# Kernel tuning notes

Measured on AMD Instinct MI355X. Metric: run time of the kernel, lower is better.

## Reference

```python
import jax, jax.numpy as jnp
import numpy as np

E = 8          # num_experts
TOP_K = 2
CAP_RATIO = 1.2


def setup_inputs() -> dict:
    key = jax.random.key(0)
    k1, k2, k3, k4 = jax.random.split(key, 4)
    B, L, D, H = 2, 2048, 768, 2048
    x = jax.random.normal(k1, (B, L, D), dtype=jnp.float32)
    Wg = jax.random.normal(k2, (D, E), dtype=jnp.float32) * 0.02   # gate: Linear(D, E, bias=False)
    W1 = jax.random.normal(k3, (E, D, 2 * H), dtype=jnp.float32) * 0.02  # fc1 per expert (y | gate halves)
    W2 = jax.random.normal(k4, (E, H, D), dtype=jnp.float32) * 0.02      # fc2 per expert
    return {"x": x, "Wg": Wg, "W1": W1, "W2": W2}


def reference(x, Wg, W1, W2):
    B, L, D = x.shape
    H = W2.shape[1]
    xf = x.reshape(-1, D)                      # [N, D]
    N = xf.shape[0]
    capacity = int(CAP_RATIO * N / E)          # static, matches torch int()

    logits = xf @ Wg                           # [N, E]
    scores, idx = jax.lax.top_k(logits, TOP_K) # [N, K] (descending, like torch.topk)
    weights = jax.nn.softmax(scores, axis=-1)  # [N, K]

    # padded token table: row N is a zero token used for unfilled capacity slots
    xpad = jnp.concatenate([xf, jnp.zeros((1, D), xf.dtype)], axis=0)
    wpad_zero = jnp.zeros((1,), weights.dtype)
    out = jnp.zeros((N, D), x.dtype)

    for k in range(TOP_K):
        ik = idx[:, k]                                         # [N] expert id per token
        onehot = (ik[:, None] == jnp.arange(E)[None, :])       # [N, E]
        pos = jnp.cumsum(onehot, axis=0) - 1                   # rank within expert, ascending token order
        posk = jnp.take_along_axis(pos, ik[:, None], axis=1)[:, 0]  # [N]
        keep = posk < capacity                                 # first-come capacity (== indices[:capacity])

        # dispatch buffer [E, C]: token index per slot, N (pad) where unfilled/dropped
        buf = jnp.full((E, capacity), N, dtype=jnp.int32)
        buf = buf.at[ik, posk].set(jnp.arange(N, dtype=jnp.int32), mode="drop")

        xg = xpad[buf]                                         # [E, C, D]
        h = jnp.einsum("ecd,edh->ech", xg, W1)                 # [E, C, 2H]
        act = h[..., :H] * jax.nn.silu(h[..., H:])             # GatedMLP: y * silu(gate)
        ye = jnp.einsum("ech,ehd->ecd", act, W2)               # [E, C, D]

        wk = jnp.where(keep, weights[:, k], 0.0)               # [N]
        w_buf = jnp.concatenate([wk, wpad_zero])[buf]          # [E, C], 0 on pad slots
        out = out.at[buf.reshape(-1)].add(
            (w_buf[..., None] * ye).reshape(E * capacity, D), mode="drop"
        )

    return out.reshape(B, L, D)
```

## Files before the change

### kernel.cpp

```cpp
#include <hip/hip_runtime.h>


typedef _Float16 half8 __attribute__((ext_vector_type(8)));
typedef _Float16 half4t __attribute__((ext_vector_type(4)));
typedef float f4 __attribute__((ext_vector_type(4)));

#define N_TOK 4096
#define DDIM  768
#define HDIM  2048
#define NEXP  8
#define CAP   614
#define CAPP  640

#define XH_OFF    0L
#define W1T_OFF   6292992L
#define W2T_OFF   56624640L
#define ACT_OFF   81790464L
#define EIDX_OFF  123733504L
#define WTS_OFF   123766272L
#define TOKL_OFF  123799040L
#define CNT_OFF   123840000L

__device__ __forceinline__ void gld16(const void* g, void* l) {
  __builtin_amdgcn_global_load_lds(
      (const __attribute__((address_space(1))) unsigned int*)g,
      (__attribute__((address_space(3))) unsigned int*)l, 16, 0, 0);
}

__global__ __launch_bounds__(256) void cvt_tr_kernel(const float* __restrict__ src,
                                                     _Float16* __restrict__ dst,
                                                     int R, int C) {
  __shared__ float tile[64 * 69];
  int e = blockIdx.z;
  int r0 = blockIdx.x * 64, c0 = blockIdx.y * 64;
  long sb = (long)e * R * C;
  int t = threadIdx.x;
  int rrow = t >> 4, c4 = (t & 15) * 4;
#pragma unroll
  for (int i = 0; i < 4; i++) {
    int row = i * 16 + rrow;
    f4 v = *(const f4*)(src + sb + (long)(r0 + row) * C + c0 + c4);
    *(f4*)(&tile[row * 69 + c4]) = v;
  }
  __syncthreads();
#pragma unroll
  for (int s = 0; s < 2; s++) {
    int idx = t + s * 256;
    int c = idx >> 3, ch = idx & 7;
    half8 h;
#pragma unroll
    for (int j = 0; j < 8; j++) h[j] = (_Float16)tile[(ch * 8 + j) * 69 + c];
    *(half8*)(dst + sb + (long)(c0 + c) * R + r0 + ch * 8) = h;
  }
}

__global__ __launch_bounds__(256) void router_kernel(const float* __restrict__ x,
                                                     const float* __restrict__ Wg,
                                                     _Float16* __restrict__ xh,
                                                     int* __restrict__ eidx,
                                                     float* __restrict__ wts) {
  __shared__ float wg[DDIM * NEXP];
  int t = threadIdx.x;
  for (int i = t; i < DDIM * NEXP; i += 256) wg[i] = Wg[i];
  __syncthreads();
  int w = t >> 6, lane = t & 63;
  int tok = blockIdx.x * 4 + w;
  if (tok > N_TOK) return;
  if (tok == N_TOK) {
    half4t zz; zz[0] = zz[1] = zz[2] = zz[3] = (_Float16)0.f;
#pragma unroll
    for (int j = 0; j < 3; j++) *(half4t*)(xh + (long)N_TOK * DDIM + (lane + j * 64) * 4) = zz;
    return;
  }
  const float* xr = x + (long)tok * DDIM;
#pragma unroll
  for (int j = 0; j < 3; j++) {
    f4 v = *(const f4*)(xr + (lane + j * 64) * 4);
    half4t hv;
    hv[0] = (_Float16)v[0]; hv[1] = (_Float16)v[1];
    hv[2] = (_Float16)v[2]; hv[3] = (_Float16)v[3];
    *(half4t*)(xh + (long)tok * DDIM + (lane + j * 64) * 4) = hv;
  }
  float acc[8] = {0.f, 0.f, 0.f, 0.f, 0.f, 0.f, 0.f, 0.f};
#pragma unroll
  for (int i = 0; i < 12; i++) {
    float xv = xr[i * 64 + lane];
    const float* wr = &wg[(i * 64 + lane) * 8];
#pragma unroll
    for (int e2 = 0; e2 < 8; e2++) acc[e2] += xv * wr[e2];
  }
#pragma unroll
  for (int e2 = 0; e2 < 8; e2++) {
    float v = acc[e2];
    v += __shfl_xor(v, 32); v += __shfl_xor(v, 16); v += __shfl_xor(v, 8);
    v += __shfl_xor(v, 4);  v += __shfl_xor(v, 2);  v += __shfl_xor(v, 1);
    acc[e2] = v;
  }
  if (lane == 0) {
    float m0 = -1e30f; int i0 = 0;
#pragma unroll
    for (int e2 = 0; e2 < 8; e2++) if (acc[e2] > m0) { m0 = acc[e2]; i0 = e2; }
    float m1 = -1e30f; int i1 = 0;
#pragma unroll
    for (int e2 = 0; e2 < 8; e2++) if (e2 != i0 && acc[e2] > m1) { m1 = acc[e2]; i1 = e2; }
    float tt = __expf(m1 - m0);
    float w0 = 1.f / (1.f + tt);
    eidx[tok * 2 + 0] = i0; eidx[tok * 2 + 1] = i1;
    wts[tok * 2 + 0] = w0;  wts[tok * 2 + 1] = 1.f - w0;
  }
}

__global__ __launch_bounds__(64) void scan_kernel(const int* __restrict__ eidx,
                                                  int* __restrict__ toklist,
                                                  int* __restrict__ counts) {
  int z = blockIdx.x;
  int k = z >> 3, e = z & 7;
  int lane = threadIdx.x;
  int mye[64];
#pragma unroll
  for (int c = 0; c < 64; c++) mye[c] = eidx[(c * 64 + lane) * 2 + k];
  int base = 0;
#pragma unroll 4
  for (int c = 0; c < 64; c++) {
    int n = c * 64 + lane;
    bool pred = (mye[c] == e);
    unsigned long long mask = __ballot(pred);
    if (pred) {
      int pos = base + __popcll(mask & ((1ull << lane) - 1ull));
      if (pos < CAP) toklist[z * CAPP + pos] = n;
    }
    base += __popcll(mask);
  }
  if (lane == 0) counts[z] = (base < CAP) ? base : CAP;
}

__global__ __launch_bounds__(256, 2) void gemm1_kernel(const _Float16* __restrict__ xh,
                                                       const _Float16* __restrict__ w1t,
                                                       const int* __restrict__ toklist,
                                                       const int* __restrict__ counts,
                                                       _Float16* __restrict__ act) {
  int i = blockIdx.x;
  int xcd = i & 7, j = i >> 3;
  int m = j % 5, ii = j / 5;
  int k = ii & 1, n = ii >> 1;
  int e = xcd, z = k * 8 + e;
  int count = counts[z];
  int m0 = m * 128;
  if (m0 >= count) return;
  int n0 = n * 128;

  __shared__ _Float16 As[128 * 64];
  __shared__ _Float16 Bs[256 * 64];
  __shared__ int toks[128];

  int t = threadIdx.x;
  if (t < 128) {
    int r = m0 + t;
    toks[t] = (r < count) ? toklist[z * CAPP + r] : N_TOK;
  }
  __syncthreads();

  int lane = t & 63, w = t >> 6;
  int l8 = lane >> 3, u8 = lane & 7;

  const _Float16* ag[4]; _Float16* al[4];
#pragma unroll
  for (int s = 0; s < 4; s++) {
    int row = w * 32 + s * 8 + l8;
    ag[s] = xh + (long)toks[row] * DDIM + ((u8 ^ (row & 7)) * 8);
    al[s] = As + row * 64 + u8 * 8;
  }
  const _Float16* bg[8]; _Float16* bl[8];
#pragma unroll
  for (int s = 0; s < 8; s++) {
    int rb = w * 64 + s * 8 + l8;
    int gr = (rb < 128) ? (n0 + rb) : (2048 + n0 + (rb - 128));
    bg[s] = w1t + ((long)e * 4096 + gr) * DDIM + ((u8 ^ (rb & 7)) * 8);
    bl[s] = Bs + rb * 64 + u8 * 8;
  }

  int q = lane >> 4, m16 = lane & 15;
  int wm = w & 1, wn = w >> 1;

  f4 zero4 = {0.f, 0.f, 0.f, 0.f};
  f4 acc[4][4][2];
#pragma unroll
  for (int rt = 0; rt < 4; rt++)
#pragma unroll
    for (int ct = 0; ct < 4; ct++) { acc[rt][ct][0] = zero4; acc[rt][ct][1] = zero4; }

  for (int kk = 0; kk < DDIM; kk += 64) {
    __syncthreads();
#pragma unroll
    for (int s = 0; s < 4; s++) { gld16(ag[s], al[s]); ag[s] += 64; }
#pragma unroll
    for (int s = 0; s < 8; s++) { gld16(bg[s], bl[s]); bg[s] += 64; }
    __syncthreads();

#pragma unroll
    for (int c = 0; c < 2; c++) {
      half8 af[4], bf[4][2];
#pragma unroll
      for (int rt = 0; rt < 4; rt++) {
        int row = wm * 64 + rt * 16 + m16;
        af[rt] = *(const half8*)(As + row * 64 + (((c * 4 + q) ^ (row & 7)) * 8));
      }
#pragma unroll
      for (int ct = 0; ct < 4; ct++) {
        int cb = wn * 64 + ct * 16 + m16;
        int ph = ((c * 4 + q) ^ (cb & 7)) * 8;
        bf[ct][0] = *(const half8*)(Bs + cb * 64 + ph);
        bf[ct][1] = *(const half8*)(Bs + (128 + cb) * 64 + ph);
      }
#pragma unroll
      for (int rt = 0; rt < 4; rt++)
#pragma unroll
        for (int ct = 0; ct < 4; ct++) {
          acc[rt][ct][0] = __builtin_amdgcn_mfma_f32_16x16x32_f16(af[rt], bf[ct][0], acc[rt][ct][0], 0, 0, 0);
          acc[rt][ct][1] = __builtin_amdgcn_mfma_f32_16x16x32_f16(af[rt], bf[ct][1], acc[rt][ct][1], 0, 0, 0);
        }
    }
  }

  long ab = (long)z * CAPP * HDIM;
#pragma unroll
  for (int rt = 0; rt < 4; rt++)
#pragma unroll
    for (int ct = 0; ct < 4; ct++)
#pragma unroll
      for (int r = 0; r < 4; r++) {
        int row = m0 + wm * 64 + rt * 16 + q * 4 + r;
        int col = n0 + wn * 64 + ct * 16 + m16;
        float h1 = acc[rt][ct][0][r], h2 = acc[rt][ct][1][r];
        float s = h2 / (1.f + __expf(-h2));
        act[ab + (long)row * HDIM + col] = (_Float16)(h1 * s);
      }
}

__global__ __launch_bounds__(256, 3) void gemm2_kernel(const _Float16* __restrict__ act,
                                                       const _Float16* __restrict__ w2t,
                                                       const int* __restrict__ toklist,
                                                       const int* __restrict__ counts,
                                                       const float* __restrict__ wts,
                                                       float* __restrict__ out) {
  int i = blockIdx.x;
  int xcd = i & 7, j = i >> 3;
  int m = j % 5, t2 = j / 5;
  int k = t2 & 1, n = t2 >> 1;
  int e = xcd, z = k * 8 + e;
  int count = counts[z];
  int m0 = m * 128;
  if (m0 >= count) return;
  int n0 = n * 128;

  __shared__ _Float16 As[128 * 64];
  __shared__ _Float16 Bs[128 * 64];
  __shared__ int toksL[128];
  __shared__ float wrow[128];

  int t = threadIdx.x;
  if (t < 128) {
    int r = m0 + t;
    if (r < count) {
      int tok = toklist[z * CAPP + r];
      toksL[t] = tok;
      wrow[t] = wts[tok * 2 + k];
    } else {
      toksL[t] = -1;
      wrow[t] = 0.f;
    }
  }
  __syncthreads();

  int lane = t & 63, w = t >> 6;
  int l8 = lane >> 3, u8 = lane & 7;

  const _Float16* ag[4]; _Float16* al[4];
#pragma unroll
  for (int s = 0; s < 4; s++) {
    int row = w * 32 + s * 8 + l8;
    ag[s] = act + ((long)z * CAPP + m0 + row) * HDIM + ((u8 ^ (row & 7)) * 8);
    al[s] = As + row * 64 + u8 * 8;
  }
  const _Float16* bg[4]; _Float16* bl[4];
#pragma unroll
  for (int s = 0; s < 4; s++) {
    int rb = w * 32 + s * 8 + l8;
    bg[s] = w2t + ((long)e * DDIM + n0 + rb) * HDIM + ((u8 ^ (rb & 7)) * 8);
    bl[s] = Bs + rb * 64 + u8 * 8;
  }

  int q = lane >> 4, m16 = lane & 15;
  int wm = w & 1, wn = w >> 1;

  f4 zero4 = {0.f, 0.f, 0.f, 0.f};
  f4 acc[4][4];
#pragma unroll
  for (int rt = 0; rt < 4; rt++)
#pragma unroll
    for (int ct = 0; ct < 4; ct++) acc[rt][ct] = zero4;

  for (int kk = 0; kk < HDIM; kk += 64) {
    __syncthreads();
#pragma unroll
    for (int s = 0; s < 4; s++) { gld16(ag[s], al[s]); ag[s] += 64; }
#pragma unroll
    for (int s = 0; s < 4; s++) { gld16(bg[s], bl[s]); bg[s] += 64; }
    __syncthreads();

#pragma unroll
    for (int c = 0; c < 2; c++) {
      half8 af[4], bf[4];
#pragma unroll
      for (int rt = 0; rt < 4; rt++) {
        int row = wm * 64 + rt * 16 + m16;
        af[rt] = *(const half8*)(As + row * 64 + (((c * 4 + q) ^ (row & 7)) * 8));
      }
#pragma unroll
      for (int ct = 0; ct < 4; ct++) {
        int cb = wn * 64 + ct * 16 + m16;
        bf[ct] = *(const half8*)(Bs + cb * 64 + (((c * 4 + q) ^ (cb & 7)) * 8));
      }
#pragma unroll
      for (int rt = 0; rt < 4; rt++)
#pragma unroll
        for (int ct = 0; ct < 4; ct++)
          acc[rt][ct] = __builtin_amdgcn_mfma_f32_16x16x32_f16(af[rt], bf[ct], acc[rt][ct], 0, 0, 0);
    }
  }

#pragma unroll
  for (int rt = 0; rt < 4; rt++)
#pragma unroll
    for (int ct = 0; ct < 4; ct++)
#pragma unroll
      for (int r = 0; r < 4; r++) {
        int lr = wm * 64 + rt * 16 + q * 4 + r;
        int tok = toksL[lr];
        if (tok >= 0) {
          int col = n0 + wn * 64 + ct * 16 + m16;
          atomicAdd(&out[(long)tok * DDIM + col], wrow[lr] * acc[rt][ct][r]);
        }
      }
}


extern "C" void kernel_launch(void* const* d_in, const int* in_sizes, int n_in,
                              void* d_out, int out_size, void* d_ws, size_t ws_size,
                              hipStream_t stream) {
  const float* x  = (const float*)d_in[0];
  const float* Wg = (const float*)d_in[1];
  const float* W1 = (const float*)d_in[2];
  const float* W2 = (const float*)d_in[3];
  float* out = (float*)d_out;
  char* ws = (char*)d_ws;

  _Float16* xh   = (_Float16*)(ws + XH_OFF);
  _Float16* w1t  = (_Float16*)(ws + W1T_OFF);
  _Float16* w2t  = (_Float16*)(ws + W2T_OFF);
  _Float16* actb = (_Float16*)(ws + ACT_OFF);
  int* eidx      = (int*)(ws + EIDX_OFF);
  float* wts     = (float*)(ws + WTS_OFF);
  int* toklist   = (int*)(ws + TOKL_OFF);
  int* counts    = (int*)(ws + CNT_OFF);

  hipMemsetAsync(d_out, 0, (size_t)out_size * sizeof(float), stream);
  cvt_tr_kernel<<<dim3(12, 64, 8), 256, 0, stream>>>(W1, w1t, 768, 4096);
  cvt_tr_kernel<<<dim3(32, 12, 8), 256, 0, stream>>>(W2, w2t, 2048, 768);
  router_kernel<<<1025, 256, 0, stream>>>(x, Wg, xh, eidx, wts);
  scan_kernel<<<16, 64, 0, stream>>>(eidx, toklist, counts);
  gemm1_kernel<<<1280, 256, 0, stream>>>(xh, w1t, toklist, counts, actb);
  gemm2_kernel<<<480, 256, 0, stream>>>(actb, w2t, toklist, counts, wts, out);
}
```

Measured before the change: 349.2 us.

## Double-buffer LDS and enlarge tiles in expert GEMMs with 512-thread blocks

Both expert GEMMs move to 512-thread blocks with larger tiles: 256x128 for gemm1 with the y and gate halves interleaved, and 128x256 for gemm2. Global-to-LDS loads are double-buffered with explicit vmcnt waits and raw s_barriers, and MFMA sections get raised priority. The aim is to overlap memory loads with MFMA work and raise data reuse per block. The router also transposes the gate weights in shared memory to avoid bank conflicts. In exchange, each block holds more registers and LDS, and the hand-written waitcnt and barrier ordering is fragile if the load counts change.

```diff
diff --git a/kernel.cpp b/kernel.cpp
--- a/kernel.cpp
+++ b/kernel.cpp
@@ -59,9 +59,9 @@
                                                      _Float16* __restrict__ xh,
                                                      int* __restrict__ eidx,
                                                      float* __restrict__ wts) {
-  __shared__ float wg[DDIM * NEXP];
+  __shared__ float wgT[NEXP * DDIM];
   int t = threadIdx.x;
-  for (int i = t; i < DDIM * NEXP; i += 256) wg[i] = Wg[i];
+  for (int i = t; i < DDIM * NEXP; i += 256) wgT[(i & 7) * DDIM + (i >> 3)] = Wg[i];
   __syncthreads();
   int w = t >> 6, lane = t & 63;
   int tok = blockIdx.x * 4 + w;
@@ -85,9 +85,8 @@
 #pragma unroll
   for (int i = 0; i < 12; i++) {
     float xv = xr[i * 64 + lane];
-    const float* wr = &wg[(i * 64 + lane) * 8];
-#pragma unroll
-    for (int e2 = 0; e2 < 8; e2++) acc[e2] += xv * wr[e2];
+#pragma unroll
+    for (int e2 = 0; e2 < 8; e2++) acc[e2] += xv * wgT[e2 * DDIM + i * 64 + lane];
   }
 #pragma unroll
   for (int e2 = 0; e2 < 8; e2++) {
@@ -134,127 +133,154 @@
   if (lane == 0) counts[z] = (base < CAP) ? base : CAP;
 }
 
-__global__ __launch_bounds__(256, 2) void gemm1_kernel(const _Float16* __restrict__ xh,
+__global__ __launch_bounds__(512, 2) void gemm1_kernel(const _Float16* __restrict__ xh,
                                                        const _Float16* __restrict__ w1t,
                                                        const int* __restrict__ toklist,
                                                        const int* __restrict__ counts,
                                                        _Float16* __restrict__ act) {
   int i = blockIdx.x;
-  int xcd = i & 7, j = i >> 3;
-  int m = j % 5, ii = j / 5;
-  int k = ii & 1, n = ii >> 1;
-  int e = xcd, z = k * 8 + e;
+  int e = i & 7, j = i >> 3;
+  int m = j % 3, nk = j / 3;
+  int k = nk & 1, n = nk >> 1;
+  int z = k * 8 + e;
   int count = counts[z];
-  int m0 = m * 128;
+  int m0 = m * 256;
   if (m0 >= count) return;
   int n0 = n * 128;
 
-  __shared__ _Float16 As[128 * 64];
-  __shared__ _Float16 Bs[256 * 64];
-  __shared__ int toks[128];
+  __shared__ _Float16 lds[2][32768];
 
   int t = threadIdx.x;
-  if (t < 128) {
-    int r = m0 + t;
-    toks[t] = (r < count) ? toklist[z * CAPP + r] : N_TOK;
-  }
-  __syncthreads();
-
-  int lane = t & 63, w = t >> 6;
-  int l8 = lane >> 3, u8 = lane & 7;
-
-  const _Float16* ag[4]; _Float16* al[4];
+  int u = t & 7, rg = t >> 3;
+  int swz = (u ^ (rg & 7)) * 8;
+
+  int tokr[4];
 #pragma unroll
   for (int s = 0; s < 4; s++) {
-    int row = w * 32 + s * 8 + l8;
-    ag[s] = xh + (long)toks[row] * DDIM + ((u8 ^ (row & 7)) * 8);
-    al[s] = As + row * 64 + u8 * 8;
-  }
-  const _Float16* bg[8]; _Float16* bl[8];
-#pragma unroll
-  for (int s = 0; s < 8; s++) {
-    int rb = w * 64 + s * 8 + l8;
-    int gr = (rb < 128) ? (n0 + rb) : (2048 + n0 + (rb - 128));
-    bg[s] = w1t + ((long)e * 4096 + gr) * DDIM + ((u8 ^ (rb & 7)) * 8);
-    bl[s] = Bs + rb * 64 + u8 * 8;
-  }
-
+    int r = m0 + s * 64 + rg;
+    tokr[s] = (r < count) ? toklist[z * CAPP + r] : N_TOK;
+  }
+
+  const _Float16* ag[4];
+  const _Float16* bg[4];
+  int adst[4], bdst[4];
+#pragma unroll
+  for (int s = 0; s < 4; s++) {
+    int row = s * 64 + rg;
+    ag[s] = xh + (long)tokr[s] * DDIM + swz;
+    adst[s] = row * 64 + u * 8;
+    int rb = row;
+    int hc = n0 + ((rb >> 6) << 5) + (rb & 31) + ((rb >> 5) & 1) * 2048;
+    bg[s] = w1t + ((long)e * 4096 + hc) * DDIM + swz;
+    bdst[s] = 16384 + rb * 64 + u * 8;
+  }
+
+  int lane = t & 63, wid = t >> 6;
+  int wm = wid >> 2, wn = wid & 3;
   int q = lane >> 4, m16 = lane & 15;
-  int wm = w & 1, wn = w >> 1;
 
   f4 zero4 = {0.f, 0.f, 0.f, 0.f};
-  f4 acc[4][4][2];
-#pragma unroll
-  for (int rt = 0; rt < 4; rt++)
-#pragma unroll
-    for (int ct = 0; ct < 4; ct++) { acc[rt][ct][0] = zero4; acc[rt][ct][1] = zero4; }
-
-  for (int kk = 0; kk < DDIM; kk += 64) {
-    __syncthreads();
-#pragma unroll
-    for (int s = 0; s < 4; s++) { gld16(ag[s], al[s]); ag[s] += 64; }
-#pragma unroll
-    for (int s = 0; s < 8; s++) { gld16(bg[s], bl[s]); bg[s] += 64; }
-    __syncthreads();
-
-#pragma unroll
-    for (int c = 0; c < 2; c++) {
-      half8 af[4], bf[4][2];
-#pragma unroll
-      for (int rt = 0; rt < 4; rt++) {
-        int row = wm * 64 + rt * 16 + m16;
-        af[rt] = *(const half8*)(As + row * 64 + (((c * 4 + q) ^ (row & 7)) * 8));
-      }
+  f4 acc[8][4];
+#pragma unroll
+  for (int mt = 0; mt < 8; mt++)
+#pragma unroll
+    for (int ct = 0; ct < 4; ct++) acc[mt][ct] = zero4;
+
+  asm volatile("s_waitcnt vmcnt(0)" ::: "memory");
+  __builtin_amdgcn_sched_barrier(0);
+
+#pragma unroll
+  for (int s = 0; s < 4; s++) gld16(ag[s], &lds[0][adst[s]]);
+#pragma unroll
+  for (int s = 0; s < 4; s++) gld16(bg[s], &lds[0][bdst[s]]);
+#pragma unroll
+  for (int s = 0; s < 4; s++) gld16(ag[s] + 64, &lds[1][adst[s]]);
+#pragma unroll
+  for (int s = 0; s < 4; s++) gld16(bg[s] + 64, &lds[1][bdst[s]]);
+#pragma unroll
+  for (int s = 0; s < 4; s++) { ag[s] += 128; bg[s] += 128; }
+
+  for (int t2 = 0; t2 < 12; t2++) {
+    int p = t2 & 1;
+    const _Float16* A = &lds[p][0];
+    const _Float16* B = &lds[p][16384];
+    if (t2 < 11) { asm volatile("s_waitcnt vmcnt(8)" ::: "memory"); }
+    else         { asm volatile("s_waitcnt vmcnt(0)" ::: "memory"); }
+    __builtin_amdgcn_sched_barrier(0);
+    __builtin_amdgcn_s_barrier();
+    __builtin_amdgcn_sched_barrier(0);
+
+#pragma unroll
+    for (int kk = 0; kk < 2; kk++) {
+      half8 bfr[4];
 #pragma unroll
       for (int ct = 0; ct < 4; ct++) {
-        int cb = wn * 64 + ct * 16 + m16;
-        int ph = ((c * 4 + q) ^ (cb & 7)) * 8;
-        bf[ct][0] = *(const half8*)(Bs + cb * 64 + ph);
-        bf[ct][1] = *(const half8*)(Bs + (128 + cb) * 64 + ph);
-      }
-#pragma unroll
-      for (int rt = 0; rt < 4; rt++)
-#pragma unroll
-        for (int ct = 0; ct < 4; ct++) {
-          acc[rt][ct][0] = __builtin_amdgcn_mfma_f32_16x16x32_f16(af[rt], bf[ct][0], acc[rt][ct][0], 0, 0, 0);
-          acc[rt][ct][1] = __builtin_amdgcn_mfma_f32_16x16x32_f16(af[rt], bf[ct][1], acc[rt][ct][1], 0, 0, 0);
+        int rb = wn * 64 + ct * 16 + m16;
+        bfr[ct] = *(const half8*)(B + rb * 64 + (((kk * 4 + q) ^ (rb & 7)) * 8));
+      }
+      __builtin_amdgcn_s_setprio(1);
+#pragma unroll
+      for (int mt = 0; mt < 8; mt++) {
+        int row = wm * 128 + mt * 16 + m16;
+        half8 a = *(const half8*)(A + row * 64 + (((kk * 4 + q) ^ (row & 7)) * 8));
+#pragma unroll
+        for (int ct = 0; ct < 4; ct++)
+          acc[mt][ct] = __builtin_amdgcn_mfma_f32_16x16x32_f16(a, bfr[ct], acc[mt][ct], 0, 0, 0);
+      }
+      __builtin_amdgcn_s_setprio(0);
+    }
+    asm volatile("s_waitcnt lgkmcnt(0)" ::: "memory");
+    __builtin_amdgcn_sched_barrier(0);
+    __builtin_amdgcn_s_barrier();
+    __builtin_amdgcn_sched_barrier(0);
+    if (t2 < 10) {
+#pragma unroll
+      for (int s = 0; s < 4; s++) gld16(ag[s], &lds[p][adst[s]]);
+#pragma unroll
+      for (int s = 0; s < 4; s++) gld16(bg[s], &lds[p][bdst[s]]);
+#pragma unroll
+      for (int s = 0; s < 4; s++) { ag[s] += 64; bg[s] += 64; }
+    }
+    __builtin_amdgcn_sched_barrier(0);
+  }
+
+  long ab = (long)z * CAPP * HDIM;
+#pragma unroll
+  for (int mt = 0; mt < 8; mt++) {
+    int row0 = m0 + wm * 128 + mt * 16 + q * 4;
+#pragma unroll
+    for (int cp = 0; cp < 2; cp++) {
+      int col = n0 + wn * 32 + cp * 16 + m16;
+#pragma unroll
+      for (int r = 0; r < 4; r++) {
+        int row = row0 + r;
+        if (row < CAPP) {
+          float h1 = acc[mt][cp][r], h2 = acc[mt][2 + cp][r];
+          float s = h2 / (1.f + __expf(-h2));
+          act[ab + (long)row * HDIM + col] = (_Float16)(h1 * s);
         }
-    }
-  }
-
-  long ab = (long)z * CAPP * HDIM;
-#pragma unroll
-  for (int rt = 0; rt < 4; rt++)
-#pragma unroll
-    for (int ct = 0; ct < 4; ct++)
-#pragma unroll
-      for (int r = 0; r < 4; r++) {
-        int row = m0 + wm * 64 + rt * 16 + q * 4 + r;
-        int col = n0 + wn * 64 + ct * 16 + m16;
-        float h1 = acc[rt][ct][0][r], h2 = acc[rt][ct][1][r];
-        float s = h2 / (1.f + __expf(-h2));
-        act[ab + (long)row * HDIM + col] = (_Float16)(h1 * s);
-      }
-}
-
-__global__ __launch_bounds__(256, 3) void gemm2_kernel(const _Float16* __restrict__ act,
+      }
+    }
+  }
+}
+
+__global__ __launch_bounds__(512, 2) void gemm2_kernel(const _Float16* __restrict__ act,
                                                        const _Float16* __restrict__ w2t,
                                                        const int* __restrict__ toklist,
                                                        const int* __restrict__ counts,
                                                        const float* __restrict__ wts,
                                                        float* __restrict__ out) {
   int i = blockIdx.x;
-  int xcd = i & 7, j = i >> 3;
-  int m = j % 5, t2 = j / 5;
-  int k = t2 & 1, n = t2 >> 1;
-  int e = xcd, z = k * 8 + e;
+  int e = i & 7, j = i >> 3;
+  int m = j % 5, nk = j / 5;
+  int k = nk & 1, n = nk >> 1;
+  int z = k * 8 + e;
   int count = counts[z];
   int m0 = m * 128;
   if (m0 >= count) return;
-  int n0 = n * 128;
-
-  __shared__ _Float16 As[128 * 64];
-  __shared__ _Float16 Bs[128 * 64];
+  int n0 = n * 256;
+
+  __shared__ _Float16 lds[2][24576];
   __shared__ int toksL[128];
   __shared__ float wrow[128];
 
@@ -272,74 +298,106 @@
   }
   __syncthreads();
 
-  int lane = t & 63, w = t >> 6;
-  int l8 = lane >> 3, u8 = lane & 7;
-
-  const _Float16* ag[4]; _Float16* al[4];
+  int u = t & 7, rg = t >> 3;
+  int swz = (u ^ (rg & 7)) * 8;
+
+  const _Float16* ag[2];
+  const _Float16* bg[4];
+  int adst[2], bdst[4];
+#pragma unroll
+  for (int s = 0; s < 2; s++) {
+    int row = s * 64 + rg;
+    ag[s] = act + ((long)z * CAPP + m0 + row) * HDIM + swz;
+    adst[s] = row * 64 + u * 8;
+  }
 #pragma unroll
   for (int s = 0; s < 4; s++) {
-    int row = w * 32 + s * 8 + l8;
-    ag[s] = act + ((long)z * CAPP + m0 + row) * HDIM + ((u8 ^ (row & 7)) * 8);
-    al[s] = As + row * 64 + u8 * 8;
-  }
-  const _Float16* bg[4]; _Float16* bl[4];
-#pragma unroll
-  for (int s = 0; s < 4; s++) {
-    int rb = w * 32 + s * 8 + l8;
-    bg[s] = w2t + ((long)e * DDIM + n0 + rb) * HDIM + ((u8 ^ (rb & 7)) * 8);
-    bl[s] = Bs + rb * 64 + u8 * 8;
-  }
-
+    int rb = s * 64 + rg;
+    bg[s] = w2t + ((long)e * DDIM + n0 + rb) * HDIM + swz;
+    bdst[s] = 8192 + rb * 64 + u * 8;
+  }
+
+  int lane = t & 63, wid = t >> 6;
+  int wm = wid >> 2, wn = wid & 3;
   int q = lane >> 4, m16 = lane & 15;
-  int wm = w & 1, wn = w >> 1;
 
   f4 zero4 = {0.f, 0.f, 0.f, 0.f};
   f4 acc[4][4];
 #pragma unroll
-  for (int rt = 0; rt < 4; rt++)
-#pragma unroll
-    for (int ct = 0; ct < 4; ct++) acc[rt][ct] = zero4;
-
-  for (int kk = 0; kk < HDIM; kk += 64) {
-    __syncthreads();
-#pragma unroll
-    for (int s = 0; s < 4; s++) { gld16(ag[s], al[s]); ag[s] += 64; }
-#pragma unroll
-    for (int s = 0; s < 4; s++) { gld16(bg[s], bl[s]); bg[s] += 64; }
-    __syncthreads();
-
-#pragma unroll
-    for (int c = 0; c < 2; c++) {
-      half8 af[4], bf[4];
-#pragma unroll
-      for (int rt = 0; rt < 4; rt++) {
-        int row = wm * 64 + rt * 16 + m16;
-        af[rt] = *(const half8*)(As + row * 64 + (((c * 4 + q) ^ (row & 7)) * 8));
-      }
+  for (int mt = 0; mt < 4; mt++)
+#pragma unroll
+    for (int ct = 0; ct < 4; ct++) acc[mt][ct] = zero4;
+
+#pragma unroll
+  for (int s = 0; s < 2; s++) gld16(ag[s], &lds[0][adst[s]]);
+#pragma unroll
+  for (int s = 0; s < 4; s++) gld16(bg[s], &lds[0][bdst[s]]);
+#pragma unroll
+  for (int s = 0; s < 2; s++) gld16(ag[s] + 64, &lds[1][adst[s]]);
+#pragma unroll
+  for (int s = 0; s < 4; s++) gld16(bg[s] + 64, &lds[1][bdst[s]]);
+#pragma unroll
+  for (int s = 0; s < 2; s++) ag[s] += 128;
+#pragma unroll
+  for (int s = 0; s < 4; s++) bg[s] += 128;
+
+  for (int t2 = 0; t2 < 32; t2++) {
+    int p = t2 & 1;
+    const _Float16* A = &lds[p][0];
+    const _Float16* B = &lds[p][8192];
+    if (t2 < 31) { asm volatile("s_waitcnt vmcnt(6)" ::: "memory"); }
+    else         { asm volatile("s_waitcnt vmcnt(0)" ::: "memory"); }
+    __builtin_amdgcn_sched_barrier(0);
+    __builtin_amdgcn_s_barrier();
+    __builtin_amdgcn_sched_barrier(0);
+
+#pragma unroll
+    for (int kk = 0; kk < 2; kk++) {
+      half8 bfr[4];
 #pragma unroll
       for (int ct = 0; ct < 4; ct++) {
-        int cb = wn * 64 + ct * 16 + m16;
-        bf[ct] = *(const half8*)(Bs + cb * 64 + (((c * 4 + q) ^ (cb & 7)) * 8));
-      }
-#pragma unroll
-      for (int rt = 0; rt < 4; rt++)
+        int rb = wn * 64 + ct * 16 + m16;
+        bfr[ct] = *(const half8*)(B + rb * 64 + (((kk * 4 + q) ^ (rb & 7)) * 8));
+      }
+      __builtin_amdgcn_s_setprio(1);
+#pragma unroll
+      for (int mt = 0; mt < 4; mt++) {
+        int row = wm * 64 + mt * 16 + m16;
+        half8 a = *(const half8*)(A + row * 64 + (((kk * 4 + q) ^ (row & 7)) * 8));
 #pragma unroll
         for (int ct = 0; ct < 4; ct++)
-          acc[rt][ct] = __builtin_amdgcn_mfma_f32_16x16x32_f16(af[rt], bf[ct], acc[rt][ct], 0, 0, 0);
-    }
-  }
-
-#pragma unroll
-  for (int rt = 0; rt < 4; rt++)
+          acc[mt][ct] = __builtin_amdgcn_mfma_f32_16x16x32_f16(a, bfr[ct], acc[mt][ct], 0, 0, 0);
+      }
+      __builtin_amdgcn_s_setprio(0);
+    }
+    asm volatile("s_waitcnt lgkmcnt(0)" ::: "memory");
+    __builtin_amdgcn_sched_barrier(0);
+    __builtin_amdgcn_s_barrier();
+    __builtin_amdgcn_sched_barrier(0);
+    if (t2 < 30) {
+#pragma unroll
+      for (int s = 0; s < 2; s++) gld16(ag[s], &lds[p][adst[s]]);
+#pragma unroll
+      for (int s = 0; s < 4; s++) gld16(bg[s], &lds[p][bdst[s]]);
+#pragma unroll
+      for (int s = 0; s < 2; s++) ag[s] += 64;
+#pragma unroll
+      for (int s = 0; s < 4; s++) bg[s] += 64;
+    }
+    __builtin_amdgcn_sched_barrier(0);
+  }
+
+#pragma unroll
+  for (int mt = 0; mt < 4; mt++)
 #pragma unroll
     for (int ct = 0; ct < 4; ct++)
 #pragma unroll
       for (int r = 0; r < 4; r++) {
-        int lr = wm * 64 + rt * 16 + q * 4 + r;
+        int lr = wm * 64 + mt * 16 + q * 4 + r;
         int tok = toksL[lr];
         if (tok >= 0) {
           int col = n0 + wn * 64 + ct * 16 + m16;
-          atomicAdd(&out[(long)tok * DDIM + col], wrow[lr] * acc[rt][ct][r]);
+          atomicAdd(&out[(long)tok * DDIM + col], wrow[lr] * acc[mt][ct][r]);
         }
       }
 }
@@ -369,6 +427,6 @@
   cvt_tr_kernel<<<dim3(32, 12, 8), 256, 0, stream>>>(W2, w2t, 2048, 768);
   router_kernel<<<1025, 256, 0, stream>>>(x, Wg, xh, eidx, wts);
   scan_kernel<<<16, 64, 0, stream>>>(eidx, toklist, counts);
-  gemm1_kernel<<<1280, 256, 0, stream>>>(xh, w1t, toklist, counts, actb);
-  gemm2_kernel<<<480, 256, 0, stream>>>(actb, w2t, toklist, counts, wts, out);
-}
+  gemm1_kernel<<<768, 512, 0, stream>>>(xh, w1t, toklist, counts, actb);
+  gemm2_kernel<<<240, 512, 0, stream>>>(actb, w2t, toklist, counts, wts, out);
+}
```

New measurement: 369.3 us. +5.8%, slower.
